# Performance work log

Measured on AMD Instinct MI355X. Metric: run time of the kernel, lower is better.

Reference implementation:

```python
import jax, jax.numpy as jnp
import numpy as np

NUM_HEADS = 16

def setup_inputs() -> dict:
    key = jax.random.key(0)
    ks = jax.random.split(key, 7)
    B, N, D = 2, 2048, 1024
    x = jax.random.normal(ks[0], (B, N, D), dtype=jnp.float32)
    gamma = jax.random.uniform(ks[1], (B, NUM_HEADS), dtype=jnp.float32)
    dist_matrix = jax.random.uniform(ks[2], (N, N), dtype=jnp.float32)
    W_qkv = jax.random.normal(ks[3], (D, 3 * D), dtype=jnp.float32) * (D ** -0.5)
    b_qkv = jnp.zeros((3 * D,), dtype=jnp.float32)
    W_proj = jax.random.normal(ks[4], (D, D), dtype=jnp.float32) * (D ** -0.5)
    b_proj = jnp.zeros((D,), dtype=jnp.float32)
    return {"x": x, "gamma": gamma, "dist_matrix": dist_matrix,
            "W_qkv": W_qkv, "b_qkv": b_qkv, "W_proj": W_proj, "b_proj": b_proj}

def reference(x, gamma, dist_matrix, W_qkv, b_qkv, W_proj, b_proj):
    B, N, D = x.shape
    H = NUM_HEADS
    hd = D // H
    scale = D ** -0.5  # standard_scale=False -> dim**-0.5
    # qkv projection: [B,N,3D] -> [3,B,H,N,hd]
    qkv = (x @ W_qkv + b_qkv).reshape(B, N, 3, H, hd).transpose(2, 0, 3, 1, 4)
    q, k, v = qkv[0], qkv[1], qkv[2]
    # scores with zoom bias: [B,H,N,N]
    scores = jnp.einsum('bhnd,bhmd->bhnm', q, k) * scale
    scores = scores - gamma[:, :, None, None] * dist_matrix[None, None, :, :]
    attn = jax.nn.softmax(scores, axis=-1)
    out = jnp.einsum('bhnm,bhmd->bhnd', attn, v)  # [B,H,N,hd]
    out = out.transpose(0, 2, 1, 3).reshape(B, N, D)
    return out @ W_proj + b_proj
```

## Files before the change

kernel.cpp:

```cpp
#include <hip/hip_runtime.h>
#include <cstdint>
#include <cstddef>

#define HD 64
#define NH 16
#define BATCH 2
#define SEQ 2048
#define DIM 1024
#define SCALE 0.03125f
#define LOG2E 1.4426950408889634f
#define QSCALE (SCALE * LOG2E)
#define PST 72
#define NT (SEQ / 64)

typedef short bf16x8 __attribute__((ext_vector_type(8)));
typedef float f32x4 __attribute__((ext_vector_type(4)));

#define GL16(gp, lp) __builtin_amdgcn_global_load_lds( \
    (const __attribute__((address_space(1))) unsigned int*)(gp), \
    (__attribute__((address_space(3))) unsigned int*)(lp), 16, 0, 0)

static __device__ __forceinline__ unsigned short f2bf(float f) {
  union { float f; unsigned u; } a; a.f = f;
  unsigned r = a.u + 0x7fffu + ((a.u >> 16) & 1u);
  return (unsigned short)(r >> 16);
}

static __device__ __forceinline__ f32x4 zero4() {
  f32x4 z; z[0] = 0.f; z[1] = 0.f; z[2] = 0.f; z[3] = 0.f; return z;
}

__global__ void convert_x(const float* __restrict__ in, unsigned short* __restrict__ out, int n4) {
  int i = blockIdx.x * blockDim.x + threadIdx.x;
  if (i < n4) {
    float4 v = reinterpret_cast<const float4*>(in)[i];
    ushort4 o;
    o.x = f2bf(v.x); o.y = f2bf(v.y); o.z = f2bf(v.z); o.w = f2bf(v.w);
    reinterpret_cast<ushort4*>(out)[i] = o;
  }
}

__global__ void transpose_convert(const float* __restrict__ in, unsigned short* __restrict__ out,
                                  int R, int C) {
  __shared__ float tile[32][33];
  int bx = blockIdx.x * 32;
  int by = blockIdx.y * 32;
  int tx = threadIdx.x, ty = threadIdx.y;
  #pragma unroll
  for (int i = 0; i < 32; i += 8)
    tile[ty + i][tx] = in[(size_t)(by + ty + i) * C + bx + tx];
  __syncthreads();
  #pragma unroll
  for (int i = 0; i < 32; i += 8)
    out[(size_t)(bx + ty + i) * R + by + tx] = f2bf(tile[tx][ty + i]);
}

__global__ __launch_bounds__(256) void gemm_bt(
    const unsigned short* __restrict__ A, const unsigned short* __restrict__ Bt,
    const float* __restrict__ bias, int K, int mode,
    unsigned short* __restrict__ qo, unsigned short* __restrict__ ko,
    unsigned short* __restrict__ vo, float* __restrict__ outf) {
  __shared__ __attribute__((aligned(16))) unsigned short As[64][72];
  __shared__ __attribute__((aligned(16))) unsigned short Bs[64][72];
  int tid = threadIdx.x;
  int lane = tid & 63;
  int w = tid >> 6;
  int wm = w >> 1, wn = w & 1;
  int m0 = blockIdx.y * 64, n0 = blockIdx.x * 64;
  int r0 = tid >> 3, c0 = (tid & 7) * 8;

  f32x4 acc[2][2];
  #pragma unroll
  for (int mr = 0; mr < 2; ++mr)
    #pragma unroll
    for (int nr = 0; nr < 2; ++nr) acc[mr][nr] = zero4();

  int nkt = K / 64;
  for (int kt = 0; kt < nkt; ++kt) {
    int k0 = kt * 64;
    uint4 a0 = *reinterpret_cast<const uint4*>(&A[(size_t)(m0 + r0) * K + k0 + c0]);
    uint4 a1 = *reinterpret_cast<const uint4*>(&A[(size_t)(m0 + r0 + 32) * K + k0 + c0]);
    uint4 b0 = *reinterpret_cast<const uint4*>(&Bt[(size_t)(n0 + r0) * K + k0 + c0]);
    uint4 b1 = *reinterpret_cast<const uint4*>(&Bt[(size_t)(n0 + r0 + 32) * K + k0 + c0]);
    *reinterpret_cast<uint4*>(&As[r0][c0]) = a0;
    *reinterpret_cast<uint4*>(&As[r0 + 32][c0]) = a1;
    *reinterpret_cast<uint4*>(&Bs[r0][c0]) = b0;
    *reinterpret_cast<uint4*>(&Bs[r0 + 32][c0]) = b1;
    __syncthreads();
    #pragma unroll
    for (int kc = 0; kc < 2; ++kc) {
      bf16x8 af[2], bfr[2];
      #pragma unroll
      for (int mr = 0; mr < 2; ++mr)
        af[mr] = *reinterpret_cast<const bf16x8*>(
            &As[wm * 32 + mr * 16 + (lane & 15)][kc * 32 + (lane >> 4) * 8]);
      #pragma unroll
      for (int nr = 0; nr < 2; ++nr)
        bfr[nr] = *reinterpret_cast<const bf16x8*>(
            &Bs[wn * 32 + nr * 16 + (lane & 15)][kc * 32 + (lane >> 4) * 8]);
      #pragma unroll
      for (int mr = 0; mr < 2; ++mr)
        #pragma unroll
        for (int nr = 0; nr < 2; ++nr)
          acc[mr][nr] = __builtin_amdgcn_mfma_f32_16x16x32_bf16(af[mr], bfr[nr], acc[mr][nr], 0, 0, 0);
    }
    __syncthreads();
  }

  #pragma unroll
  for (int mr = 0; mr < 2; ++mr)
    #pragma unroll
    for (int nr = 0; nr < 2; ++nr)
      #pragma unroll
      for (int j = 0; j < 4; ++j) {
        int grow = m0 + wm * 32 + mr * 16 + (lane >> 4) * 4 + j;
        int gcol = n0 + wn * 32 + nr * 16 + (lane & 15);
        float val = acc[mr][nr][j] + bias[gcol];
        if (mode == 0) {
          int which = gcol >> 10;
          int hh = (gcol >> 6) & 15;
          int d = gcol & 63;
          int bb = grow >> 11;
          int n = grow & 2047;
          if (which == 0) {
            qo[((size_t)(bb * NH + hh) * SEQ + n) * HD + d] = f2bf(val * QSCALE);
          } else if (which == 1) {
            ko[((size_t)(bb * NH + hh) * SEQ + n) * HD + d] = f2bf(val);
          } else {
            vo[((size_t)(bb * NH + hh) * HD + d) * SEQ + n] = f2bf(val);
          }
        } else {
          outf[(size_t)grow * DIM + gcol] = val;
        }
      }
}

__global__ __launch_bounds__(256, 2) void attn_kernel(
    const unsigned short* __restrict__ qb, const unsigned short* __restrict__ kb,
    const unsigned short* __restrict__ vtb, const float* __restrict__ gamma,
    const float* __restrict__ dist, unsigned short* __restrict__ ab) {
  __shared__ __attribute__((aligned(16))) unsigned short Ks[2][64][64];
  __shared__ __attribute__((aligned(16))) unsigned short Vt[2][64][64];
  __shared__ __attribute__((aligned(16))) unsigned short Ps[4][32][PST];
  const int tid = threadIdx.x;
  const int lane = tid & 63;
  const int w = tid >> 6;
  const int lo = lane & 15;
  const int hi = lane >> 4;
  const int idx = blockIdx.x;
  const int bh = idx & 31;
  const int qt = idx >> 5;
  const int b = bh >> 4, h = bh & 15;
  const int qrow0 = qt * 128 + w * 32;
  const float g2 = gamma[bh] * LOG2E;

  const size_t base = (size_t)bh * SEQ * HD;
  const size_t vtbase = (size_t)bh * HD * SEQ;

  bf16x8 qf[2][2];
  #pragma unroll
  for (int qs = 0; qs < 2; ++qs)
    #pragma unroll
    for (int kc = 0; kc < 2; ++kc)
      qf[qs][kc] = *reinterpret_cast<const bf16x8*>(
          &qb[base + (size_t)(qrow0 + qs * 16 + lo) * HD + kc * 32 + hi * 8]);

  const float* drow0 = dist + (size_t)(qrow0 + lo) * SEQ + hi * 4;
  const float* drow1 = drow0 + (size_t)16 * SEQ;

  f32x4 o[2][4];
  #pragma unroll
  for (int qs = 0; qs < 2; ++qs)
    #pragma unroll
    for (int db = 0; db < 4; ++db) o[qs][db] = zero4();
  float m_run[2] = {-INFINITY, -INFINITY};
  float l_run[2] = {0.f, 0.f};

  const int srow = tid >> 3;
  const int schunk = (tid & 7) ^ (srow & 7);
  const unsigned short* ksrc0 = kb + base + (size_t)srow * HD + schunk * 8;
  const unsigned short* ksrc1 = ksrc0 + (size_t)32 * HD;
  const unsigned short* vsrc0 = vtb + vtbase + (size_t)srow * SEQ + schunk * 8;
  const unsigned short* vsrc1 = vsrc0 + (size_t)32 * SEQ;

  GL16(ksrc0, &Ks[0][w * 8][0]);
  GL16(ksrc1, &Ks[0][32 + w * 8][0]);
  GL16(vsrc0, &Vt[0][w * 8][0]);
  GL16(vsrc1, &Vt[0][32 + w * 8][0]);
  f32x4 dvc[2][4], dvn[2][4];
  #pragma unroll
  for (int nb = 0; nb < 4; ++nb) {
    dvc[0][nb] = *reinterpret_cast<const f32x4*>(drow0 + nb * 16);
    dvc[1][nb] = *reinterpret_cast<const f32x4*>(drow1 + nb * 16);
  }
  __syncthreads();

  for (int mt = 0; mt < NT; ++mt) {
    const int cur = mt & 1;
    if (mt + 1 < NT) {
      const int m1 = (mt + 1) * 64;
      GL16(ksrc0 + (size_t)m1 * HD, &Ks[cur ^ 1][w * 8][0]);
      GL16(ksrc1 + (size_t)m1 * HD, &Ks[cur ^ 1][32 + w * 8][0]);
      GL16(vsrc0 + m1, &Vt[cur ^ 1][w * 8][0]);
      GL16(vsrc1 + m1, &Vt[cur ^ 1][32 + w * 8][0]);
      #pragma unroll
      for (int nb = 0; nb < 4; ++nb) {
        dvn[0][nb] = *reinterpret_cast<const f32x4*>(drow0 + m1 + nb * 16);
        dvn[1][nb] = *reinterpret_cast<const f32x4*>(drow1 + m1 + nb * 16);
      }
    }

    f32x4 s[2][4];
    #pragma unroll
    for (int qs = 0; qs < 2; ++qs)
      #pragma unroll
      for (int nb = 0; nb < 4; ++nb) s[qs][nb] = zero4();
    __builtin_amdgcn_s_setprio(1);
    #pragma unroll
    for (int nb = 0; nb < 4; ++nb)
      #pragma unroll
      for (int kc = 0; kc < 2; ++kc) {
        bf16x8 kf = *reinterpret_cast<const bf16x8*>(
            &Ks[cur][nb * 16 + lo][((kc * 4 + hi) ^ (lo & 7)) * 8]);
        #pragma unroll
        for (int qs = 0; qs < 2; ++qs)
          s[qs][nb] = __builtin_amdgcn_mfma_f32_16x16x32_bf16(kf, qf[qs][kc], s[qs][nb], 0, 0, 0);
      }
    __builtin_amdgcn_s_setprio(0);

    #pragma unroll
    for (int qs = 0; qs < 2; ++qs) {
      float pm = -INFINITY;
      #pragma unroll
      for (int nb = 0; nb < 4; ++nb)
        #pragma unroll
        for (int j = 0; j < 4; ++j) {
          float v = __builtin_fmaf(-g2, dvc[qs][nb][j], s[qs][nb][j]);
          s[qs][nb][j] = v;
          pm = fmaxf(pm, v);
        }
      pm = fmaxf(pm, __shfl_xor(pm, 16, 64));
      pm = fmaxf(pm, __shfl_xor(pm, 32, 64));
      float mn = fmaxf(m_run[qs], pm);
      float corr = exp2f(m_run[qs] - mn);
      m_run[qs] = mn;
      float psum = 0.f;
      #pragma unroll
      for (int nb = 0; nb < 4; ++nb) {
        float p0 = exp2f(s[qs][nb][0] - mn);
        float p1 = exp2f(s[qs][nb][1] - mn);
        float p2 = exp2f(s[qs][nb][2] - mn);
        float p3 = exp2f(s[qs][nb][3] - mn);
        psum += (p0 + p1) + (p2 + p3);
        ushort4 pw;
        pw.x = f2bf(p0); pw.y = f2bf(p1); pw.z = f2bf(p2); pw.w = f2bf(p3);
        *reinterpret_cast<ushort4*>(&Ps[w][qs * 16 + lo][nb * 16 + hi * 4]) = pw;
      }
      psum += __shfl_xor(psum, 16, 64);
      psum += __shfl_xor(psum, 32, 64);
      l_run[qs] = l_run[qs] * corr + psum;
      #pragma unroll
      for (int db = 0; db < 4; ++db) {
        o[qs][db][0] *= corr; o[qs][db][1] *= corr;
        o[qs][db][2] *= corr; o[qs][db][3] *= corr;
      }
    }

    __builtin_amdgcn_s_setprio(1);
    #pragma unroll
    for (int kc = 0; kc < 2; ++kc) {
      bf16x8 pf[2];
      #pragma unroll
      for (int qs = 0; qs < 2; ++qs)
        pf[qs] = *reinterpret_cast<const bf16x8*>(
            &Ps[w][qs * 16 + lo][kc * 32 + hi * 8]);
      #pragma unroll
      for (int db = 0; db < 4; ++db) {
        bf16x8 vtf = *reinterpret_cast<const bf16x8*>(
            &Vt[cur][db * 16 + lo][((kc * 4 + hi) ^ (lo & 7)) * 8]);
        #pragma unroll
        for (int qs = 0; qs < 2; ++qs)
          o[qs][db] = __builtin_amdgcn_mfma_f32_16x16x32_bf16(vtf, pf[qs], o[qs][db], 0, 0, 0);
      }
    }
    __builtin_amdgcn_s_setprio(0);

    if (mt + 1 < NT) {
      #pragma unroll
      for (int qs = 0; qs < 2; ++qs)
        #pragma unroll
        for (int nb = 0; nb < 4; ++nb) dvc[qs][nb] = dvn[qs][nb];
    }
    __syncthreads();
  }

  #pragma unroll
  for (int qs = 0; qs < 2; ++qs) {
    float rl = 1.0f / l_run[qs];
    size_t row = (size_t)b * SEQ + qrow0 + qs * 16 + lo;
    #pragma unroll
    for (int db = 0; db < 4; ++db) {
      ushort4 w4;
      w4.x = f2bf(o[qs][db][0] * rl);
      w4.y = f2bf(o[qs][db][1] * rl);
      w4.z = f2bf(o[qs][db][2] * rl);
      w4.w = f2bf(o[qs][db][3] * rl);
      *reinterpret_cast<ushort4*>(&ab[row * DIM + h * HD + db * 16 + hi * 4]) = w4;
    }
  }
}

extern "C" void kernel_launch(void* const* d_in, const int* in_sizes, int n_in,
                              void* d_out, int out_size, void* d_ws, size_t ws_size,
                              hipStream_t stream) {
  const float* x     = (const float*)d_in[0];
  const float* gamma = (const float*)d_in[1];
  const float* dist  = (const float*)d_in[2];
  const float* Wqkv  = (const float*)d_in[3];
  const float* bqkv  = (const float*)d_in[4];
  const float* Wproj = (const float*)d_in[5];
  const float* bproj = (const float*)d_in[6];
  float* out = (float*)d_out;

  char* ws = (char*)d_ws;
  unsigned short* xb     = (unsigned short*)(ws);
  unsigned short* wqkvt  = (unsigned short*)(ws + 8388608);
  unsigned short* wprojt = (unsigned short*)(ws + 14680064);
  unsigned short* qbuf   = (unsigned short*)(ws + 16777216);
  unsigned short* kbuf   = (unsigned short*)(ws + 25165824);
  unsigned short* vtbuf  = (unsigned short*)(ws + 33554432);
  unsigned short* abuf   = (unsigned short*)(ws + 41943040);

  convert_x<<<4096, 256, 0, stream>>>(x, xb, (BATCH * SEQ * DIM) / 4);
  transpose_convert<<<dim3(96, 32), dim3(32, 8), 0, stream>>>(Wqkv, wqkvt, DIM, 3 * DIM);
  transpose_convert<<<dim3(32, 32), dim3(32, 8), 0, stream>>>(Wproj, wprojt, DIM, DIM);
  gemm_bt<<<dim3(48, 64), 256, 0, stream>>>(xb, wqkvt, bqkv, DIM, 0, qbuf, kbuf, vtbuf, nullptr);
  attn_kernel<<<(SEQ / 128) * BATCH * NH, 256, 0, stream>>>(qbuf, kbuf, vtbuf, gamma, dist, abuf);
  gemm_bt<<<dim3(16, 64), 256, 0, stream>>>(abuf, wprojt, bproj, DIM, 1, nullptr, nullptr, nullptr, out);
}
```

Baseline: 199.4 us.

## Enlarge GEMM tiles, shrink attention query tile, add lazy rescale and packed bf16 P

The GEMM moves to 128x128 tiles with a 4x4 MFMA grid per wave, filled by direct global-to-LDS loads and raised wave priority, to increase operand reuse and cut load instructions. The attention kernel now gives each wave 16 query rows instead of 32, doubling block count and allowing 4 blocks per CU. It also skips the running-max rescale unless the max grows by more than 8 (log2 units), packs P to bf16 with v_cvt_pk_bf16_f32 into an XOR-swizzled LDS buffer, and unrolls the tile loop twice to drop the double-buffer copies of dist values. The risks are lower MFMA reuse per wave in attention, more traffic for K/V and dist per query row, and larger GEMM tiles leaving fewer blocks for the projection GEMM.

```diff
diff --git a/kernel.cpp b/kernel.cpp
--- a/kernel.cpp
+++ b/kernel.cpp
@@ -10,11 +10,12 @@
 #define SCALE 0.03125f
 #define LOG2E 1.4426950408889634f
 #define QSCALE (SCALE * LOG2E)
-#define PST 72
 #define NT (SEQ / 64)
 
 typedef short bf16x8 __attribute__((ext_vector_type(8)));
 typedef float f32x4 __attribute__((ext_vector_type(4)));
+typedef unsigned u32x2 __attribute__((ext_vector_type(2)));
+typedef unsigned u32x4 __attribute__((ext_vector_type(4)));
 
 #define GL16(gp, lp) __builtin_amdgcn_global_load_lds( \
     (const __attribute__((address_space(1))) unsigned int*)(gp), \
@@ -55,67 +56,70 @@
     out[(size_t)(bx + ty + i) * R + by + tx] = f2bf(tile[tx][ty + i]);
 }
 
-__global__ __launch_bounds__(256) void gemm_bt(
+__global__ __launch_bounds__(256) void gemm128(
     const unsigned short* __restrict__ A, const unsigned short* __restrict__ Bt,
     const float* __restrict__ bias, int K, int mode,
     unsigned short* __restrict__ qo, unsigned short* __restrict__ ko,
     unsigned short* __restrict__ vo, float* __restrict__ outf) {
-  __shared__ __attribute__((aligned(16))) unsigned short As[64][72];
-  __shared__ __attribute__((aligned(16))) unsigned short Bs[64][72];
-  int tid = threadIdx.x;
-  int lane = tid & 63;
-  int w = tid >> 6;
-  int wm = w >> 1, wn = w & 1;
-  int m0 = blockIdx.y * 64, n0 = blockIdx.x * 64;
-  int r0 = tid >> 3, c0 = (tid & 7) * 8;
-
-  f32x4 acc[2][2];
-  #pragma unroll
-  for (int mr = 0; mr < 2; ++mr)
-    #pragma unroll
-    for (int nr = 0; nr < 2; ++nr) acc[mr][nr] = zero4();
-
-  int nkt = K / 64;
+  __shared__ __attribute__((aligned(16))) unsigned short As[128 * 64];
+  __shared__ __attribute__((aligned(16))) unsigned short Bs[128 * 64];
+  const int tid = threadIdx.x;
+  const int lane = tid & 63, w = tid >> 6;
+  const int lo = lane & 15, hi = lane >> 4;
+  const int wm = w >> 1, wn = w & 1;
+  const int m0 = blockIdx.y * 128, n0 = blockIdx.x * 128;
+  const int srow = tid >> 3, scol = (tid & 7) * 8;
+  const unsigned short* abase = A + (size_t)(m0 + srow) * K + scol;
+  const unsigned short* bbase = Bt + (size_t)(n0 + srow) * K + scol;
+
+  f32x4 acc[4][4];
+  #pragma unroll
+  for (int mr = 0; mr < 4; ++mr)
+    #pragma unroll
+    for (int nr = 0; nr < 4; ++nr) acc[mr][nr] = zero4();
+
+  const int nkt = K / 64;
   for (int kt = 0; kt < nkt; ++kt) {
-    int k0 = kt * 64;
-    uint4 a0 = *reinterpret_cast<const uint4*>(&A[(size_t)(m0 + r0) * K + k0 + c0]);
-    uint4 a1 = *reinterpret_cast<const uint4*>(&A[(size_t)(m0 + r0 + 32) * K + k0 + c0]);
-    uint4 b0 = *reinterpret_cast<const uint4*>(&Bt[(size_t)(n0 + r0) * K + k0 + c0]);
-    uint4 b1 = *reinterpret_cast<const uint4*>(&Bt[(size_t)(n0 + r0 + 32) * K + k0 + c0]);
-    *reinterpret_cast<uint4*>(&As[r0][c0]) = a0;
-    *reinterpret_cast<uint4*>(&As[r0 + 32][c0]) = a1;
-    *reinterpret_cast<uint4*>(&Bs[r0][c0]) = b0;
-    *reinterpret_cast<uint4*>(&Bs[r0 + 32][c0]) = b1;
+    const unsigned short* ak = abase + kt * 64;
+    const unsigned short* bk = bbase + kt * 64;
+    #pragma unroll
+    for (int i = 0; i < 4; ++i) {
+      GL16(ak + (size_t)(32 * i) * K, &As[(w * 64 + 256 * i) * 8]);
+      GL16(bk + (size_t)(32 * i) * K, &Bs[(w * 64 + 256 * i) * 8]);
+    }
     __syncthreads();
+    __builtin_amdgcn_s_setprio(1);
     #pragma unroll
     for (int kc = 0; kc < 2; ++kc) {
-      bf16x8 af[2], bfr[2];
+      bf16x8 af[4], bfr[4];
       #pragma unroll
-      for (int mr = 0; mr < 2; ++mr)
+      for (int mr = 0; mr < 4; ++mr)
         af[mr] = *reinterpret_cast<const bf16x8*>(
-            &As[wm * 32 + mr * 16 + (lane & 15)][kc * 32 + (lane >> 4) * 8]);
+            &As[(wm * 64 + mr * 16 + lo) * 64 + kc * 32 + hi * 8]);
       #pragma unroll
-      for (int nr = 0; nr < 2; ++nr)
+      for (int nr = 0; nr < 4; ++nr)
         bfr[nr] = *reinterpret_cast<const bf16x8*>(
-            &Bs[wn * 32 + nr * 16 + (lane & 15)][kc * 32 + (lane >> 4) * 8]);
+            &Bs[(wn * 64 + nr * 16 + lo) * 64 + kc * 32 + hi * 8]);
       #pragma unroll
-      for (int mr = 0; mr < 2; ++mr)
+      for (int mr = 0; mr < 4; ++mr)
         #pragma unroll
-        for (int nr = 0; nr < 2; ++nr)
+        for (int nr = 0; nr < 4; ++nr)
           acc[mr][nr] = __builtin_amdgcn_mfma_f32_16x16x32_bf16(af[mr], bfr[nr], acc[mr][nr], 0, 0, 0);
     }
+    __builtin_amdgcn_s_setprio(0);
     __syncthreads();
   }
 
   #pragma unroll
-  for (int mr = 0; mr < 2; ++mr)
-    #pragma unroll
-    for (int nr = 0; nr < 2; ++nr)
+  for (int nr = 0; nr < 4; ++nr) {
+    const int gcol = n0 + wn * 64 + nr * 16 + lo;
+    const float bv = bias[gcol];
+    #pragma unroll
+    for (int mr = 0; mr < 4; ++mr)
       #pragma unroll
       for (int j = 0; j < 4; ++j) {
-        int grow = m0 + wm * 32 + mr * 16 + (lane >> 4) * 4 + j;
-        int gcol = n0 + wn * 32 + nr * 16 + (lane & 15);
-        float val = acc[mr][nr][j] + bias[gcol];
+        const int grow = m0 + wm * 64 + mr * 16 + hi * 4 + j;
+        float val = acc[mr][nr][j] + bv;
         if (mode == 0) {
           int which = gcol >> 10;
           int hh = (gcol >> 6) & 15;
@@ -133,15 +137,16 @@
           outf[(size_t)grow * DIM + gcol] = val;
         }
       }
-}
-
-__global__ __launch_bounds__(256, 2) void attn_kernel(
+  }
+}
+
+__global__ __launch_bounds__(256, 4) void attn_kernel(
     const unsigned short* __restrict__ qb, const unsigned short* __restrict__ kb,
     const unsigned short* __restrict__ vtb, const float* __restrict__ gamma,
     const float* __restrict__ dist, unsigned short* __restrict__ ab) {
-  __shared__ __attribute__((aligned(16))) unsigned short Ks[2][64][64];
-  __shared__ __attribute__((aligned(16))) unsigned short Vt[2][64][64];
-  __shared__ __attribute__((aligned(16))) unsigned short Ps[4][32][PST];
+  __shared__ __attribute__((aligned(16))) unsigned short Ks[2][64 * 64];
+  __shared__ __attribute__((aligned(16))) unsigned short Vt[2][64 * 64];
+  __shared__ __attribute__((aligned(16))) unsigned short Ps[4 * 16 * 64];
   const int tid = threadIdx.x;
   const int lane = tid & 63;
   const int w = tid >> 6;
@@ -151,30 +156,25 @@
   const int bh = idx & 31;
   const int qt = idx >> 5;
   const int b = bh >> 4, h = bh & 15;
-  const int qrow0 = qt * 128 + w * 32;
+  const int qrow0 = qt * 64 + w * 16;
   const float g2 = gamma[bh] * LOG2E;
 
   const size_t base = (size_t)bh * SEQ * HD;
   const size_t vtbase = (size_t)bh * HD * SEQ;
 
-  bf16x8 qf[2][2];
-  #pragma unroll
-  for (int qs = 0; qs < 2; ++qs)
-    #pragma unroll
-    for (int kc = 0; kc < 2; ++kc)
-      qf[qs][kc] = *reinterpret_cast<const bf16x8*>(
-          &qb[base + (size_t)(qrow0 + qs * 16 + lo) * HD + kc * 32 + hi * 8]);
-
-  const float* drow0 = dist + (size_t)(qrow0 + lo) * SEQ + hi * 4;
-  const float* drow1 = drow0 + (size_t)16 * SEQ;
-
-  f32x4 o[2][4];
-  #pragma unroll
-  for (int qs = 0; qs < 2; ++qs)
-    #pragma unroll
-    for (int db = 0; db < 4; ++db) o[qs][db] = zero4();
-  float m_run[2] = {-INFINITY, -INFINITY};
-  float l_run[2] = {0.f, 0.f};
+  bf16x8 qf[2];
+  #pragma unroll
+  for (int kc = 0; kc < 2; ++kc)
+    qf[kc] = *reinterpret_cast<const bf16x8*>(
+        &qb[base + (size_t)(qrow0 + lo) * HD + kc * 32 + hi * 8]);
+
+  const float* drow = dist + (size_t)(qrow0 + lo) * SEQ + hi * 4;
+
+  f32x4 o[4];
+  #pragma unroll
+  for (int db = 0; db < 4; ++db) o[db] = zero4();
+  float m_run = -INFINITY;
+  float l_run = 0.f;
 
   const int srow = tid >> 3;
   const int schunk = (tid & 7) ^ (srow & 7);
@@ -183,128 +183,117 @@
   const unsigned short* vsrc0 = vtb + vtbase + (size_t)srow * SEQ + schunk * 8;
   const unsigned short* vsrc1 = vsrc0 + (size_t)32 * SEQ;
 
-  GL16(ksrc0, &Ks[0][w * 8][0]);
-  GL16(ksrc1, &Ks[0][32 + w * 8][0]);
-  GL16(vsrc0, &Vt[0][w * 8][0]);
-  GL16(vsrc1, &Vt[0][32 + w * 8][0]);
-  f32x4 dvc[2][4], dvn[2][4];
-  #pragma unroll
-  for (int nb = 0; nb < 4; ++nb) {
-    dvc[0][nb] = *reinterpret_cast<const f32x4*>(drow0 + nb * 16);
-    dvc[1][nb] = *reinterpret_cast<const f32x4*>(drow1 + nb * 16);
-  }
+  unsigned short* const psw = &Ps[w * 1024 + lo * 64];
+
+  f32x4 dvA[4], dvB[4];
+
+  GL16(ksrc0, &Ks[0][w * 512]);
+  GL16(ksrc1, &Ks[0][2048 + w * 512]);
+  GL16(vsrc0, &Vt[0][w * 512]);
+  GL16(vsrc1, &Vt[0][2048 + w * 512]);
+  #pragma unroll
+  for (int nb = 0; nb < 4; ++nb)
+    dvA[nb] = *reinterpret_cast<const f32x4*>(drow + nb * 16);
   __syncthreads();
 
-  for (int mt = 0; mt < NT; ++mt) {
-    const int cur = mt & 1;
-    if (mt + 1 < NT) {
-      const int m1 = (mt + 1) * 64;
-      GL16(ksrc0 + (size_t)m1 * HD, &Ks[cur ^ 1][w * 8][0]);
-      GL16(ksrc1 + (size_t)m1 * HD, &Ks[cur ^ 1][32 + w * 8][0]);
-      GL16(vsrc0 + m1, &Vt[cur ^ 1][w * 8][0]);
-      GL16(vsrc1 + m1, &Vt[cur ^ 1][32 + w * 8][0]);
-      #pragma unroll
-      for (int nb = 0; nb < 4; ++nb) {
-        dvn[0][nb] = *reinterpret_cast<const f32x4*>(drow0 + m1 + nb * 16);
-        dvn[1][nb] = *reinterpret_cast<const f32x4*>(drow1 + m1 + nb * 16);
-      }
-    }
-
-    f32x4 s[2][4];
-    #pragma unroll
-    for (int qs = 0; qs < 2; ++qs)
-      #pragma unroll
-      for (int nb = 0; nb < 4; ++nb) s[qs][nb] = zero4();
-    __builtin_amdgcn_s_setprio(1);
-    #pragma unroll
-    for (int nb = 0; nb < 4; ++nb)
-      #pragma unroll
-      for (int kc = 0; kc < 2; ++kc) {
-        bf16x8 kf = *reinterpret_cast<const bf16x8*>(
-            &Ks[cur][nb * 16 + lo][((kc * 4 + hi) ^ (lo & 7)) * 8]);
-        #pragma unroll
-        for (int qs = 0; qs < 2; ++qs)
-          s[qs][nb] = __builtin_amdgcn_mfma_f32_16x16x32_bf16(kf, qf[qs][kc], s[qs][nb], 0, 0, 0);
-      }
-    __builtin_amdgcn_s_setprio(0);
-
-    #pragma unroll
-    for (int qs = 0; qs < 2; ++qs) {
-      float pm = -INFINITY;
-      #pragma unroll
-      for (int nb = 0; nb < 4; ++nb)
-        #pragma unroll
-        for (int j = 0; j < 4; ++j) {
-          float v = __builtin_fmaf(-g2, dvc[qs][nb][j], s[qs][nb][j]);
-          s[qs][nb][j] = v;
-          pm = fmaxf(pm, v);
-        }
-      pm = fmaxf(pm, __shfl_xor(pm, 16, 64));
-      pm = fmaxf(pm, __shfl_xor(pm, 32, 64));
-      float mn = fmaxf(m_run[qs], pm);
-      float corr = exp2f(m_run[qs] - mn);
-      m_run[qs] = mn;
-      float psum = 0.f;
-      #pragma unroll
-      for (int nb = 0; nb < 4; ++nb) {
-        float p0 = exp2f(s[qs][nb][0] - mn);
-        float p1 = exp2f(s[qs][nb][1] - mn);
-        float p2 = exp2f(s[qs][nb][2] - mn);
-        float p3 = exp2f(s[qs][nb][3] - mn);
-        psum += (p0 + p1) + (p2 + p3);
-        ushort4 pw;
-        pw.x = f2bf(p0); pw.y = f2bf(p1); pw.z = f2bf(p2); pw.w = f2bf(p3);
-        *reinterpret_cast<ushort4*>(&Ps[w][qs * 16 + lo][nb * 16 + hi * 4]) = pw;
-      }
-      psum += __shfl_xor(psum, 16, 64);
-      psum += __shfl_xor(psum, 32, 64);
-      l_run[qs] = l_run[qs] * corr + psum;
-      #pragma unroll
-      for (int db = 0; db < 4; ++db) {
-        o[qs][db][0] *= corr; o[qs][db][1] *= corr;
-        o[qs][db][2] *= corr; o[qs][db][3] *= corr;
-      }
-    }
-
-    __builtin_amdgcn_s_setprio(1);
-    #pragma unroll
-    for (int kc = 0; kc < 2; ++kc) {
-      bf16x8 pf[2];
-      #pragma unroll
-      for (int qs = 0; qs < 2; ++qs)
-        pf[qs] = *reinterpret_cast<const bf16x8*>(
-            &Ps[w][qs * 16 + lo][kc * 32 + hi * 8]);
-      #pragma unroll
-      for (int db = 0; db < 4; ++db) {
-        bf16x8 vtf = *reinterpret_cast<const bf16x8*>(
-            &Vt[cur][db * 16 + lo][((kc * 4 + hi) ^ (lo & 7)) * 8]);
-        #pragma unroll
-        for (int qs = 0; qs < 2; ++qs)
-          o[qs][db] = __builtin_amdgcn_mfma_f32_16x16x32_bf16(vtf, pf[qs], o[qs][db], 0, 0, 0);
-      }
-    }
-    __builtin_amdgcn_s_setprio(0);
-
-    if (mt + 1 < NT) {
-      #pragma unroll
-      for (int qs = 0; qs < 2; ++qs)
-        #pragma unroll
-        for (int nb = 0; nb < 4; ++nb) dvc[qs][nb] = dvn[qs][nb];
-    }
-    __syncthreads();
-  }
-
-  #pragma unroll
-  for (int qs = 0; qs < 2; ++qs) {
-    float rl = 1.0f / l_run[qs];
-    size_t row = (size_t)b * SEQ + qrow0 + qs * 16 + lo;
+#define TILE_BODY(CUR, NXT, MT, DVC, DVN)                                              \
+  {                                                                                    \
+    if ((MT) + 1 < NT) {                                                               \
+      const int m1_ = ((MT) + 1) * 64;                                                 \
+      GL16(ksrc0 + (size_t)m1_ * HD, &Ks[NXT][w * 512]);                               \
+      GL16(ksrc1 + (size_t)m1_ * HD, &Ks[NXT][2048 + w * 512]);                        \
+      GL16(vsrc0 + m1_, &Vt[NXT][w * 512]);                                            \
+      GL16(vsrc1 + m1_, &Vt[NXT][2048 + w * 512]);                                     \
+      _Pragma("unroll")                                                                \
+      for (int nb = 0; nb < 4; ++nb)                                                   \
+        DVN[nb] = *reinterpret_cast<const f32x4*>(drow + m1_ + nb * 16);               \
+    }                                                                                  \
+    f32x4 s[4];                                                                        \
+    _Pragma("unroll")                                                                  \
+    for (int nb = 0; nb < 4; ++nb) s[nb] = zero4();                                    \
+    __builtin_amdgcn_s_setprio(1);                                                     \
+    _Pragma("unroll")                                                                  \
+    for (int nb = 0; nb < 4; ++nb)                                                     \
+      _Pragma("unroll")                                                                \
+      for (int kc = 0; kc < 2; ++kc) {                                                 \
+        bf16x8 kf = *reinterpret_cast<const bf16x8*>(                                  \
+            &Ks[CUR][(nb * 16 + lo) * 64 + ((kc * 4 + hi) ^ (lo & 7)) * 8]);           \
+        s[nb] = __builtin_amdgcn_mfma_f32_16x16x32_bf16(kf, qf[kc], s[nb], 0, 0, 0);   \
+      }                                                                                \
+    __builtin_amdgcn_s_setprio(0);                                                     \
+    float pm = -INFINITY;                                                              \
+    _Pragma("unroll")                                                                  \
+    for (int nb = 0; nb < 4; ++nb)                                                     \
+      _Pragma("unroll")                                                                \
+      for (int j = 0; j < 4; ++j) {                                                    \
+        float v_ = __builtin_fmaf(-g2, DVC[nb][j], s[nb][j]);                          \
+        s[nb][j] = v_;                                                                 \
+        pm = fmaxf(pm, v_);                                                            \
+      }                                                                                \
+    pm = fmaxf(pm, __shfl_xor(pm, 16, 64));                                            \
+    pm = fmaxf(pm, __shfl_xor(pm, 32, 64));                                            \
+    if (!__all(pm <= m_run + 8.0f)) {                                                  \
+      float mn_ = fmaxf(m_run, pm);                                                    \
+      float corr_ = exp2f(m_run - mn_);                                                \
+      m_run = mn_;                                                                     \
+      l_run *= corr_;                                                                  \
+      _Pragma("unroll")                                                                \
+      for (int db = 0; db < 4; ++db) {                                                 \
+        o[db][0] *= corr_; o[db][1] *= corr_;                                          \
+        o[db][2] *= corr_; o[db][3] *= corr_;                                          \
+      }                                                                                \
+    }                                                                                  \
+    float psum = 0.f;                                                                  \
+    _Pragma("unroll")                                                                  \
+    for (int nb = 0; nb < 4; ++nb) {                                                   \
+      float p0 = exp2f(s[nb][0] - m_run);                                              \
+      float p1 = exp2f(s[nb][1] - m_run);                                              \
+      float p2 = exp2f(s[nb][2] - m_run);                                              \
+      float p3 = exp2f(s[nb][3] - m_run);                                              \
+      psum += (p0 + p1) + (p2 + p3);                                                   \
+      unsigned pk0, pk1;                                                               \
+      asm("v_cvt_pk_bf16_f32 %0, %1, %2" : "=v"(pk0) : "v"(p0), "v"(p1));              \
+      asm("v_cvt_pk_bf16_f32 %0, %1, %2" : "=v"(pk1) : "v"(p2), "v"(p3));              \
+      u32x2 pw_; pw_[0] = pk0; pw_[1] = pk1;                                           \
+      *reinterpret_cast<u32x2*>(&psw[(((nb << 2) + hi) ^ lo) * 4]) = pw_;              \
+    }                                                                                  \
+    psum += __shfl_xor(psum, 16, 64);                                                  \
+    psum += __shfl_xor(psum, 32, 64);                                                  \
+    l_run += psum;                                                                     \
+    __builtin_amdgcn_s_setprio(1);                                                     \
+    _Pragma("unroll")                                                                  \
+    for (int kc = 0; kc < 2; ++kc) {                                                   \
+      u32x2 ra = *reinterpret_cast<const u32x2*>(&psw[(((kc << 3) + hi * 2) ^ lo) * 4]); \
+      u32x2 rb = *reinterpret_cast<const u32x2*>(&psw[(((kc << 3) + hi * 2 + 1) ^ lo) * 4]); \
+      u32x4 t_; t_[0] = ra[0]; t_[1] = ra[1]; t_[2] = rb[0]; t_[3] = rb[1];            \
+      bf16x8 pf = __builtin_bit_cast(bf16x8, t_);                                      \
+      _Pragma("unroll")                                                                \
+      for (int db = 0; db < 4; ++db) {                                                 \
+        bf16x8 vtf = *reinterpret_cast<const bf16x8*>(                                 \
+            &Vt[CUR][(db * 16 + lo) * 64 + ((kc * 4 + hi) ^ (lo & 7)) * 8]);           \
+        o[db] = __builtin_amdgcn_mfma_f32_16x16x32_bf16(vtf, pf, o[db], 0, 0, 0);      \
+      }                                                                                \
+    }                                                                                  \
+    __builtin_amdgcn_s_setprio(0);                                                     \
+    __syncthreads();                                                                   \
+  }
+
+  for (int mt = 0; mt < NT; mt += 2) {
+    TILE_BODY(0, 1, mt, dvA, dvB)
+    TILE_BODY(1, 0, mt + 1, dvB, dvA)
+  }
+#undef TILE_BODY
+
+  {
+    float rl = 1.0f / l_run;
+    size_t row = (size_t)b * SEQ + qrow0 + lo;
     #pragma unroll
     for (int db = 0; db < 4; ++db) {
       ushort4 w4;
-      w4.x = f2bf(o[qs][db][0] * rl);
-      w4.y = f2bf(o[qs][db][1] * rl);
-      w4.z = f2bf(o[qs][db][2] * rl);
-      w4.w = f2bf(o[qs][db][3] * rl);
+      w4.x = f2bf(o[db][0] * rl);
+      w4.y = f2bf(o[db][1] * rl);
+      w4.z = f2bf(o[db][2] * rl);
+      w4.w = f2bf(o[db][3] * rl);
       *reinterpret_cast<ushort4*>(&ab[row * DIM + h * HD + db * 16 + hi * 4]) = w4;
     }
   }
@@ -334,7 +323,7 @@
   convert_x<<<4096, 256, 0, stream>>>(x, xb, (BATCH * SEQ * DIM) / 4);
   transpose_convert<<<dim3(96, 32), dim3(32, 8), 0, stream>>>(Wqkv, wqkvt, DIM, 3 * DIM);
   transpose_convert<<<dim3(32, 32), dim3(32, 8), 0, stream>>>(Wproj, wprojt, DIM, DIM);
-  gemm_bt<<<dim3(48, 64), 256, 0, stream>>>(xb, wqkvt, bqkv, DIM, 0, qbuf, kbuf, vtbuf, nullptr);
-  attn_kernel<<<(SEQ / 128) * BATCH * NH, 256, 0, stream>>>(qbuf, kbuf, vtbuf, gamma, dist, abuf);
-  gemm_bt<<<dim3(16, 64), 256, 0, stream>>>(abuf, wprojt, bproj, DIM, 1, nullptr, nullptr, nullptr, out);
-}
+  gemm128<<<dim3(24, 32), 256, 0, stream>>>(xb, wqkvt, bqkv, DIM, 0, qbuf, kbuf, vtbuf, nullptr);
+  attn_kernel<<<(SEQ / 64) * BATCH * NH, 256, 0, stream>>>(qbuf, kbuf, vtbuf, gamma, dist, abuf);
+  gemm128<<<dim3(8, 32), 256, 0, stream>>>(abuf, wprojt, bproj, DIM, 1, nullptr, nullptr, nullptr, out);
+}
```

Measured after the change: 172.4 us. 1.16x faster.
